# Optimization experiments

Measured on AMD Instinct MI355X. Metric: run time of the kernel, lower is better.

The kernel has to match this reference:

```python
import jax, jax.numpy as jnp
import numpy as np

N_NODES = 50000
N_EDGES = 1600000
NEG_SLOPE = 0.2


def setup_inputs() -> dict:
    key = jax.random.key(0)
    ks = jax.random.split(key, 11)
    s = 0.1  # small init scale
    return {
        "x": jax.random.normal(ks[0], (N_NODES, 128), dtype=jnp.float32),
        "edge_index": jax.random.randint(ks[1], (2, N_EDGES), 0, N_NODES, dtype=jnp.int64),
        "W1": jax.random.normal(ks[2], (128, 128), dtype=jnp.float32) * s,
        "att_src1": jax.random.normal(ks[3], (2, 64), dtype=jnp.float32) * s,
        "att_dst1": jax.random.normal(ks[4], (2, 64), dtype=jnp.float32) * s,
        "b1": jax.random.normal(ks[5], (128,), dtype=jnp.float32) * s,
        "W2": jax.random.normal(ks[6], (128, 64), dtype=jnp.float32) * s,
        "att_src2": jax.random.normal(ks[7], (1, 64), dtype=jnp.float32) * s,
        "att_dst2": jax.random.normal(ks[8], (1, 64), dtype=jnp.float32) * s,
        "b2": jax.random.normal(ks[9], (64,), dtype=jnp.float32) * s,
    }


def gat_conv(x, W, a_src, a_dst, bias, src, dst, n_nodes):
    # x: [N, F_in]; W: [F_in, H*C]; a_src/a_dst: [H, C]; bias: [H*C]
    H, C = a_src.shape
    xl = (x @ W).reshape(n_nodes, H, C)                 # [N,H,C]
    alpha_s = jnp.einsum('nhc,hc->nh', xl, a_src)       # [N,H]
    alpha_d = jnp.einsum('nhc,hc->nh', xl, a_dst)       # [N,H]
    e = jax.nn.leaky_relu(alpha_s[src] + alpha_d[dst], NEG_SLOPE)  # [E,H]
    # segment softmax over edges sharing the same destination node
    m = jax.ops.segment_max(e, dst, num_segments=n_nodes)          # [N,H]
    m = jnp.where(jnp.isfinite(m), m, 0.0)
    e = jnp.exp(e - m[dst])
    denom = jax.ops.segment_sum(e, dst, num_segments=n_nodes)      # [N,H]
    alpha = e / denom[dst]                               # self-loops guarantee denom > 0
    msg = xl[src] * alpha[:, :, None]                    # [E,H,C]
    out = jax.ops.segment_sum(msg, dst, num_segments=n_nodes)      # [N,H,C]
    return out.reshape(n_nodes, H * C) + bias


def reference(x, edge_index, W1, att_src1, att_dst1, b1, W2, att_src2, att_dst2, b2):
    n = x.shape[0]
    # PyG GATConv default add_self_loops=True
    loops = jnp.arange(n, dtype=edge_index.dtype)
    src = jnp.concatenate([edge_index[0], loops])
    dst = jnp.concatenate([edge_index[1], loops])

    h = gat_conv(x, W1, att_src1, att_dst1, b1, src, dst, n)   # [N, 128]
    h = jax.nn.relu(h)                                          # dropout p=0 (eval)
    h = gat_conv(h, W2, att_src2, att_dst2, b2, src, dst, n)   # [N, 64]
    h = jax.nn.relu(h)
    return h
```

## Files before the change

### kernel.cpp

```cpp
#include <hip/hip_runtime.h>
#include <hip/hip_fp16.h>
#include <cstdint>
#include <cstddef>

#define NEG_SLOPE 0.2f

#define NB 128
#define LOG_NB 7
#define MAXK 512

__device__ inline unsigned short f2bf(float f) {
    unsigned int u = __float_as_uint(f);
    u += 0x7FFFu + ((u >> 16) & 1u);
    return (unsigned short)(u >> 16);
}
__device__ inline float bf_lo(unsigned int u) { return __uint_as_float(u << 16); }
__device__ inline float bf_hi(unsigned int u) { return __uint_as_float(u & 0xFFFF0000u); }
__device__ inline float bfu(unsigned short u) { return __uint_as_float((unsigned int)u << 16); }
__device__ inline float lrelu(float t) { return t > 0.f ? t : NEG_SLOPE * t; }

__global__ __launch_bounds__(256) void sort_count_kernel(const int* __restrict__ ei, int E,
                                                         int K, int CH, int* __restrict__ bcnt) {
    __shared__ int hist[4 * MAXK];
    int tid = threadIdx.x;
    int wiw = tid >> 6;
    for (int i = tid; i < K; i += 256) {
        hist[i] = 0; hist[MAXK + i] = 0; hist[2 * MAXK + i] = 0; hist[3 * MAXK + i] = 0;
    }
    __syncthreads();
    int lo = blockIdx.x * CH;
    int hi = lo + CH; if (hi > E) hi = E;
    for (int e = lo + tid; e < hi; e += 256)
        atomicAdd(&hist[wiw * MAXK + (ei[(size_t)E + e] >> LOG_NB)], 1);
    __syncthreads();
    for (int i = tid; i < K; i += 256) {
        int c = hist[i] + hist[MAXK + i] + hist[2 * MAXK + i] + hist[3 * MAXK + i];
        if (c) atomicAdd(&bcnt[i], c);
    }
}

__global__ void sort_scan_kernel(const int* __restrict__ bcnt, int* __restrict__ boff,
                                 int* __restrict__ bcur, int K, int E) {
    __shared__ int buf[MAXK];
    int tid = threadIdx.x;
    int v = (tid < K) ? bcnt[tid] : 0;
    buf[tid] = v;
    __syncthreads();
    for (int o = 1; o < MAXK; o <<= 1) {
        int t = (tid >= o) ? buf[tid - o] : 0;
        __syncthreads();
        buf[tid] += t;
        __syncthreads();
    }
    if (tid < K) {
        int ex = buf[tid] - v;
        boff[tid] = ex;
        bcur[tid] = ex;
    }
    if (tid == K) boff[K] = E;
}


template <int FOUT, int H, int ROWS, bool BF16IN, bool CHUNK_OUT>
__device__ __forceinline__ void gemm_att_body(const void* __restrict__ Xv,
                                              const float* __restrict__ W,
                                              const float* __restrict__ attS,
                                              const float* __restrict__ attD,
                                              unsigned short* __restrict__ Ybf,
                                              float* __restrict__ as_,
                                              float* __restrict__ ad_, int N, int bid,
                                              float* sX, float* sW) {
    constexpr int CG  = FOUT / 4;
    constexpr int RR  = (ROWS * FOUT) / 1024;
    constexpr int LDX = 36;
    int tid = threadIdx.x;
    int rowbase = bid * ROWS;
    int cg = tid % CG;
    int rg = tid / CG;
    int r0 = rg * RR;

    float acc[RR][4];
#pragma unroll
    for (int i = 0; i < RR; i++)
#pragma unroll
        for (int c = 0; c < 4; c++) acc[i][c] = 0.f;

    for (int k0 = 0; k0 < 128; k0 += 32) {
        __syncthreads();
        for (int idx = tid; idx < ROWS * 8; idx += 256) {
            int r = idx >> 3, q = idx & 7;
            int row = rowbase + r;
            float4 val;
            if (row < N) {
                if constexpr (BF16IN) {
                    const unsigned short* Xb = (const unsigned short*)Xv;
                    ushort4 raw = *(const ushort4*)&Xb[(size_t)row * 128 + k0 + q * 4];
                    val = make_float4(bfu(raw.x), bfu(raw.y), bfu(raw.z), bfu(raw.w));
                } else {
                    const float* X = (const float*)Xv;
                    val = *(const float4*)&X[(size_t)row * 128 + k0 + q * 4];
                }
            } else {
                val = make_float4(0.f, 0.f, 0.f, 0.f);
            }
            *(float4*)&sX[r * LDX + q * 4] = val;
        }
        for (int idx = tid; idx < 8 * FOUT; idx += 256)
            *(float4*)&sW[idx * 4] = *(const float4*)&W[(size_t)k0 * FOUT + idx * 4];
        __syncthreads();
        for (int k = 0; k < 32; k += 4) {
            float4 xr[RR];
#pragma unroll
            for (int i = 0; i < RR; i++)
                xr[i] = *(const float4*)&sX[(r0 + i) * LDX + k];
#pragma unroll
            for (int kk = 0; kk < 4; kk++) {
                float4 wv = ((const float4*)(sW + (size_t)(k + kk) * FOUT))[cg];
#pragma unroll
                for (int i = 0; i < RR; i++) {
                    float xv = (&xr[i].x)[kk];
                    acc[i][0] = fmaf(xv, wv.x, acc[i][0]);
                    acc[i][1] = fmaf(xv, wv.y, acc[i][1]);
                    acc[i][2] = fmaf(xv, wv.z, acc[i][2]);
                    acc[i][3] = fmaf(xv, wv.w, acc[i][3]);
                }
            }
        }
    }

#pragma unroll
    for (int i = 0; i < RR; i++) {
        int row = rowbase + r0 + i;
        if (row < N) {
            ushort4 v;
            v.x = f2bf(acc[i][0]); v.y = f2bf(acc[i][1]);
            v.z = f2bf(acc[i][2]); v.w = f2bf(acc[i][3]);
            if constexpr (CHUNK_OUT) {
                int chunk = cg >> 3;
                int wc = (cg & 7) * 4;
                *(ushort4*)(Ybf + ((size_t)chunk * N + row) * 32 + wc) = v;
            } else {
                *(ushort4*)(Ybf + (size_t)row * FOUT + cg * 4) = v;
            }
        }
    }

    float4 asv = ((const float4*)attS)[cg];
    float4 adv = ((const float4*)attD)[cg];
    int head = (H == 2) ? (cg >> 4) : 0;
#pragma unroll
    for (int i = 0; i < RR; i++) {
        float ps = acc[i][0] * asv.x + acc[i][1] * asv.y + acc[i][2] * asv.z + acc[i][3] * asv.w;
        float pd = acc[i][0] * adv.x + acc[i][1] * adv.y + acc[i][2] * adv.z + acc[i][3] * adv.w;
#pragma unroll
        for (int o = 1; o <= 8; o <<= 1) { ps += __shfl_xor(ps, o); pd += __shfl_xor(pd, o); }
        int row = rowbase + r0 + i;
        if ((tid & 15) == 0 && row < N) {
            as_[(size_t)row * H + head] = ps;
            ad_[(size_t)row * H + head] = pd;
        }
    }
}

__global__ __launch_bounds__(256) void scatter_gemm1_kernel(const int* __restrict__ ei, int E,
                                                            int K, int CH, int* __restrict__ bcur,
                                                            unsigned int* __restrict__ bkt,
                                                            const float* __restrict__ X,
                                                            const float* __restrict__ W1,
                                                            const float* __restrict__ attS,
                                                            const float* __restrict__ attD,
                                                            unsigned short* __restrict__ Ybf,
                                                            float* __restrict__ as_,
                                                            float* __restrict__ ad_, int N, int G) {
    __shared__ float sX[64 * 36];
    __shared__ float sW[32 * 128];
    if (blockIdx.x < G) {
        int* hist = (int*)sX;
        int* base = (int*)sW;
        int* cur2 = (int*)sW + MAXK;
        int tid = threadIdx.x;
        int wiw = tid >> 6;
        for (int i = tid; i < K; i += 256) {
            hist[i] = 0; hist[MAXK + i] = 0; hist[2 * MAXK + i] = 0; hist[3 * MAXK + i] = 0;
        }
        __syncthreads();
        int lo = blockIdx.x * CH;
        int hi = lo + CH; if (hi > E) hi = E;
        for (int e = lo + tid; e < hi; e += 256)
            atomicAdd(&hist[wiw * MAXK + (ei[(size_t)E + e] >> LOG_NB)], 1);
        __syncthreads();
        for (int i = tid; i < K; i += 256) {
            int c = hist[i] + hist[MAXK + i] + hist[2 * MAXK + i] + hist[3 * MAXK + i];
            base[i] = c ? atomicAdd(&bcur[i], c) : 0;
            cur2[i] = 0;
        }
        __syncthreads();
        for (int e = lo + tid; e < hi; e += 256) {
            int s = ei[e];
            int d = ei[(size_t)E + e];
            int k = d >> LOG_NB;
            int r = atomicAdd(&cur2[k], 1);
            bkt[(size_t)base[k] + r] = (unsigned int)s | ((unsigned int)d << 16);
        }
    } else {
        gemm_att_body<128, 2, 64, false, true>(X, W1, attS, attD, Ybf, as_, ad_, N,
                                               blockIdx.x - G, sX, sW);
    }
}

__global__ __launch_bounds__(256) void gemm2_kernel(const unsigned short* __restrict__ X,
                                                    const float* __restrict__ W,
                                                    const float* __restrict__ attS,
                                                    const float* __restrict__ attD,
                                                    unsigned short* __restrict__ Ybf,
                                                    float* __restrict__ as_,
                                                    float* __restrict__ ad_, int N) {
    __shared__ float sX[64 * 36];
    __shared__ float sW[32 * 64];
    gemm_att_body<64, 1, 64, true, false>(X, W, attS, attD, Ybf, as_, ad_, N, blockIdx.x, sX, sW);
}

__global__ __launch_bounds__(256) void sort_finalize_kernel(const unsigned int* __restrict__ bkt,
                                                            const int* __restrict__ boff,
                                                            int* __restrict__ off,
                                                            unsigned int* __restrict__ csrc, int N) {
    __shared__ int nhist[4 * NB];
    __shared__ int part[256];
    __shared__ int loff[NB];
    int k = blockIdx.x;
    int tid = threadIdx.x;
    int wiw = tid >> 6;
    int node0 = k << LOG_NB;
    int nh = N - node0; if (nh > NB) nh = NB;
    int beg = boff[k], end = boff[k + 1];
    for (int i = tid; i < NB; i += 256) {
        nhist[i] = 0; nhist[NB + i] = 0; nhist[2 * NB + i] = 0; nhist[3 * NB + i] = 0;
    }
    __syncthreads();
    for (int e = beg + tid; e < end; e += 256)
        atomicAdd(&nhist[wiw * NB + ((bkt[e] >> 16) - node0)], 1);
    __syncthreads();
    int i0 = 2 * tid, i1 = 2 * tid + 1;
    int v0 = (i0 < nh) ? nhist[i0] + nhist[NB + i0] + nhist[2 * NB + i0] + nhist[3 * NB + i0] + 1 : 0;
    int v1 = (i1 < nh) ? nhist[i1] + nhist[NB + i1] + nhist[2 * NB + i1] + nhist[3 * NB + i1] + 1 : 0;
    part[tid] = v0 + v1;
    __syncthreads();
    for (int o = 1; o < 256; o <<= 1) {
        int t = (tid >= o) ? part[tid - o] : 0;
        __syncthreads();
        part[tid] += t;
        __syncthreads();
    }
    int gbase = beg + node0;
    int base = gbase + ((tid > 0) ? part[tid - 1] : 0);
    if (i0 < nh) loff[i0] = base;
    if (i1 < nh) loff[i1] = base + v0;
    __syncthreads();
    for (int i = tid; i < nh; i += 256) {
        int node = node0 + i;
        off[node] = loff[i];
        csrc[loff[i]] = (unsigned int)node | ((unsigned int)node << 16);
        nhist[i] = loff[i] + 1;
    }
    if (node0 + nh == N && tid == 0) off[N] = gbase + part[255];
    __syncthreads();
    for (int e = beg + tid; e < end; e += 256) {
        unsigned int p = bkt[e];
        int pos = atomicAdd(&nhist[(p >> 16) - node0], 1);
        csrc[pos] = p;
    }
}


__global__ __launch_bounds__(256) void alpha1_kernel(const float* __restrict__ as_,
                                                     const float* __restrict__ ad_,
                                                     const int* __restrict__ off,
                                                     const unsigned int* __restrict__ csrc,
                                                     unsigned int* __restrict__ pae0,
                                                     unsigned int* __restrict__ pae1, int N) {
    int wiw  = threadIdx.x >> 6;
    int lane = threadIdx.x & 63;
    int node = blockIdx.x * 4 + wiw;
    if (node >= N) return;
    int beg = off[node], end = off[node + 1];
    int deg = end - beg;
    float2 adn = ((const float2*)ad_)[node];
    (void)wiw;

    if (deg <= 64) {
        int s = 0;
        float t0 = -1e30f, t1 = -1e30f;
        if (lane < deg) {
            s = (int)(csrc[beg + lane] & 0xFFFFu);
            float2 asv = ((const float2*)as_)[s];
            t0 = lrelu(asv.x + adn.x);
            t1 = lrelu(asv.y + adn.y);
        }
        float m0 = t0, m1 = t1;
#pragma unroll
        for (int o = 32; o; o >>= 1) {
            m0 = fmaxf(m0, __shfl_xor(m0, o));
            m1 = fmaxf(m1, __shfl_xor(m1, o));
        }
        float e0 = (lane < deg) ? __expf(t0 - m0) : 0.f;
        float e1 = (lane < deg) ? __expf(t1 - m1) : 0.f;
        float s0 = e0, s1 = e1;
#pragma unroll
        for (int o = 32; o; o >>= 1) { s0 += __shfl_xor(s0, o); s1 += __shfl_xor(s1, o); }
        if (lane < deg) {
            unsigned int h0 = (unsigned int)__half_as_ushort(__float2half(e0 / s0));
            unsigned int h1 = (unsigned int)__half_as_ushort(__float2half(e1 / s1));
            pae0[beg + lane] = (unsigned int)s | (h0 << 16);
            pae1[beg + lane] = (unsigned int)s | (h1 << 16);
        }
    } else {
        float m0 = -1e30f, m1 = -1e30f;
        for (int b = beg; b < end; b += 64) {
            int e = b + lane;
            if (e < end) {
                int s = (int)(csrc[e] & 0xFFFFu);
                float2 asv = ((const float2*)as_)[s];
                m0 = fmaxf(m0, lrelu(asv.x + adn.x));
                m1 = fmaxf(m1, lrelu(asv.y + adn.y));
            }
        }
#pragma unroll
        for (int o = 32; o; o >>= 1) {
            m0 = fmaxf(m0, __shfl_xor(m0, o));
            m1 = fmaxf(m1, __shfl_xor(m1, o));
        }
        float s0 = 0.f, s1 = 0.f;
        for (int b = beg; b < end; b += 64) {
            int e = b + lane;
            if (e < end) {
                int s = (int)(csrc[e] & 0xFFFFu);
                float2 asv = ((const float2*)as_)[s];
                s0 += __expf(lrelu(asv.x + adn.x) - m0);
                s1 += __expf(lrelu(asv.y + adn.y) - m1);
            }
        }
#pragma unroll
        for (int o = 32; o; o >>= 1) { s0 += __shfl_xor(s0, o); s1 += __shfl_xor(s1, o); }
        float i0 = 1.f / s0, i1 = 1.f / s1;
        for (int b = beg; b < end; b += 64) {
            int e = b + lane;
            if (e < end) {
                int s = (int)(csrc[e] & 0xFFFFu);
                float2 asv = ((const float2*)as_)[s];
                float a0 = __expf(lrelu(asv.x + adn.x) - m0) * i0;
                float a1 = __expf(lrelu(asv.y + adn.y) - m1) * i1;
                unsigned int h0 = (unsigned int)__half_as_ushort(__float2half(a0));
                unsigned int h1 = (unsigned int)__half_as_ushort(__float2half(a1));
                pae0[e] = (unsigned int)s | (h0 << 16);
                pae1[e] = (unsigned int)s | (h1 << 16);
            }
        }
    }
}


__global__ __launch_bounds__(256) void chunk_agg1_kernel(const unsigned short* __restrict__ xlc,
                                                         const unsigned int* __restrict__ pae0,
                                                         const unsigned int* __restrict__ pae1,
                                                         const float* __restrict__ bias,
                                                         const int* __restrict__ off,
                                                         unsigned short* __restrict__ out,
                                                         int N) {
    int bid   = blockIdx.x;
    int slot  = bid & 7;
    int chunk = slot & 3;
    int half  = slot >> 2;
    int blkin = (bid >> 3) * 2 + half;
    int wiw   = threadIdx.x >> 6;
    int lane  = threadIdx.x & 63;
    int node  = blkin * 4 + wiw;
    if (node >= N) return;

    int beg = off[node];
    int deg = off[node + 1] - beg;
    int le = lane >> 2;
    int li = lane & 3;

    const unsigned int* pae = (chunk & 2) ? pae1 : pae0;
    const char* xb = (const char*)xlc + ((size_t)chunk * N) * 64 + li * 16;

    float acc[8];
#pragma unroll
    for (int i = 0; i < 8; i++) acc[i] = 0.f;

    int rounds = (deg + 15) >> 4;
#pragma unroll 4
    for (int r = 0; r < rounds; r++) {
        int e = r * 16 + le;
        unsigned int p = (e < deg) ? pae[beg + e] : 0u;
        float a = __half2float(__ushort_as_half((unsigned short)(p >> 16)));
        int s = (int)(p & 0xFFFFu);
        uint4 v = *(const uint4*)(xb + ((size_t)s << 6));
        acc[0] = fmaf(a, bf_lo(v.x), acc[0]); acc[1] = fmaf(a, bf_hi(v.x), acc[1]);
        acc[2] = fmaf(a, bf_lo(v.y), acc[2]); acc[3] = fmaf(a, bf_hi(v.y), acc[3]);
        acc[4] = fmaf(a, bf_lo(v.z), acc[4]); acc[5] = fmaf(a, bf_hi(v.z), acc[5]);
        acc[6] = fmaf(a, bf_lo(v.w), acc[6]); acc[7] = fmaf(a, bf_hi(v.w), acc[7]);
    }
#pragma unroll
    for (int o = 4; o <= 32; o <<= 1)
#pragma unroll
        for (int i = 0; i < 8; i++) acc[i] += __shfl_xor(acc[i], o);

    if (lane < 4) {
        const float* bp = bias + chunk * 32 + lane * 8;
        unsigned int w0 = (unsigned int)f2bf(fmaxf(acc[0] + bp[0], 0.f)) |
                          ((unsigned int)f2bf(fmaxf(acc[1] + bp[1], 0.f)) << 16);
        unsigned int w1 = (unsigned int)f2bf(fmaxf(acc[2] + bp[2], 0.f)) |
                          ((unsigned int)f2bf(fmaxf(acc[3] + bp[3], 0.f)) << 16);
        unsigned int w2 = (unsigned int)f2bf(fmaxf(acc[4] + bp[4], 0.f)) |
                          ((unsigned int)f2bf(fmaxf(acc[5] + bp[5], 0.f)) << 16);
        unsigned int w3 = (unsigned int)f2bf(fmaxf(acc[6] + bp[6], 0.f)) |
                          ((unsigned int)f2bf(fmaxf(acc[7] + bp[7], 0.f)) << 16);
        *(uint4*)(out + (size_t)node * 128 + chunk * 32 + lane * 8) = make_uint4(w0, w1, w2, w3);
    }
}


__global__ __launch_bounds__(256) void agg2_kernel(const unsigned short* __restrict__ xl,
                                                   const float* __restrict__ as_,
                                                   const float* __restrict__ ad_,
                                                   const float* __restrict__ bias,
                                                   const int* __restrict__ off,
                                                   const unsigned int* __restrict__ csrc,
                                                   float* __restrict__ out, int N) {
    __shared__ float2 sps[4][64];
    int wiw  = threadIdx.x >> 6;
    int lane = threadIdx.x & 63;
    int node = blockIdx.x * 4 + wiw;
    if (node >= N) return;
    int beg = off[node], end = off[node + 1];
    int deg = end - beg;
    float adn = ad_[node];

    int cl  = lane & 7;
    int sub = lane >> 3;
    float acc[8];
#pragma unroll
    for (int i = 0; i < 8; i++) acc[i] = 0.f;
    const char* xbase = (const char*)xl + cl * 16;

    if (deg <= 64) {
        int so = 0;
        float t = -1e30f;
        if (lane < deg) {
            int s = (int)(csrc[beg + lane] & 0xFFFFu);
            so = s << 7;
            t = as_[s] + adn;
            t = t > 0.f ? t : NEG_SLOPE * t;
        }
        float m = t;
#pragma unroll
        for (int o = 32; o; o >>= 1) m = fmaxf(m, __shfl_xor(m, o));
        float evv = (lane < deg) ? __expf(t - m) : 0.f;
        float sum = evv;
#pragma unroll
        for (int o = 32; o; o >>= 1) sum += __shfl_xor(sum, o);
        sps[wiw][lane] = make_float2(evv / sum, __int_as_float(so));
        int iters = (deg + 7) >> 3;
#pragma unroll 8
        for (int j = 0; j < iters; j++) {
            float2 q = sps[wiw][j * 8 + sub];
            float a  = q.x;
            uint4 v  = *(const uint4*)(xbase + __float_as_int(q.y));
            acc[0] = fmaf(a, bf_lo(v.x), acc[0]); acc[1] = fmaf(a, bf_hi(v.x), acc[1]);
            acc[2] = fmaf(a, bf_lo(v.y), acc[2]); acc[3] = fmaf(a, bf_hi(v.y), acc[3]);
            acc[4] = fmaf(a, bf_lo(v.z), acc[4]); acc[5] = fmaf(a, bf_hi(v.z), acc[5]);
            acc[6] = fmaf(a, bf_lo(v.w), acc[6]); acc[7] = fmaf(a, bf_hi(v.w), acc[7]);
        }
    } else {
        float m = -1e30f;
        for (int b = beg; b < end; b += 64) {
            int e = b + lane;
            if (e < end) {
                float t = as_[csrc[e] & 0xFFFFu] + adn;
                t = t > 0.f ? t : NEG_SLOPE * t;
                m = fmaxf(m, t);
            }
        }
#pragma unroll
        for (int o = 32; o; o >>= 1) m = fmaxf(m, __shfl_xor(m, o));
        float sum = 0.f;
        for (int b = beg; b < end; b += 64) {
            int e = b + lane;
            if (e < end) {
                float t = as_[csrc[e] & 0xFFFFu] + adn;
                t = t > 0.f ? t : NEG_SLOPE * t;
                sum += __expf(t - m);
            }
        }
#pragma unroll
        for (int o = 32; o; o >>= 1) sum += __shfl_xor(sum, o);
        float inv = 1.f / sum;
        for (int b = beg; b < end; b += 64) {
            int cnt = end - b; if (cnt > 64) cnt = 64;
            float p = 0.f; int so = 0;
            if (lane < cnt) {
                int s = (int)(csrc[b + lane] & 0xFFFFu);
                so = s << 7;
                float t = as_[s] + adn;
                t = t > 0.f ? t : NEG_SLOPE * t;
                p = __expf(t - m) * inv;
            }
            sps[wiw][lane] = make_float2(p, __int_as_float(so));
            int iters = (cnt + 7) >> 3;
#pragma unroll 8
            for (int j = 0; j < iters; j++) {
                float2 q = sps[wiw][j * 8 + sub];
                float a  = q.x;
                uint4 v  = *(const uint4*)(xbase + __float_as_int(q.y));
                acc[0] = fmaf(a, bf_lo(v.x), acc[0]); acc[1] = fmaf(a, bf_hi(v.x), acc[1]);
                acc[2] = fmaf(a, bf_lo(v.y), acc[2]); acc[3] = fmaf(a, bf_hi(v.y), acc[3]);
                acc[4] = fmaf(a, bf_lo(v.z), acc[4]); acc[5] = fmaf(a, bf_hi(v.z), acc[5]);
                acc[6] = fmaf(a, bf_lo(v.w), acc[6]); acc[7] = fmaf(a, bf_hi(v.w), acc[7]);
            }
        }
    }
#pragma unroll
    for (int o = 8; o <= 32; o <<= 1)
#pragma unroll
        for (int i = 0; i < 8; i++) acc[i] += __shfl_xor(acc[i], o);
    if (sub == 0) {
        float* op = out + (size_t)node * 64 + cl * 8;
        const float* bp = bias + cl * 8;
#pragma unroll
        for (int i = 0; i < 8; i++) op[i] = fmaxf(acc[i] + bp[i], 0.f);
    }
}


extern "C" void kernel_launch(void* const* d_in, const int* in_sizes, int n_in,
                              void* d_out, int out_size, void* d_ws, size_t ws_size,
                              hipStream_t stream) {
    const float* x        = (const float*)d_in[0];
    const int*   ei       = (const int*)d_in[1];
    const float* W1       = (const float*)d_in[2];
    const float* attS1    = (const float*)d_in[3];
    const float* attD1    = (const float*)d_in[4];
    const float* b1       = (const float*)d_in[5];
    const float* W2       = (const float*)d_in[6];
    const float* attS2    = (const float*)d_in[7];
    const float* attD2    = (const float*)d_in[8];
    const float* b2       = (const float*)d_in[9];
    float* out            = (float*)d_out;

    int N  = in_sizes[0] / 128;
    int E  = in_sizes[1] / 2;
    int EE = E + N;
    int K  = (N + NB - 1) >> LOG_NB;

    char* w = (char*)d_ws;
    auto alloc = [&](size_t bytes) -> void* {
        void* p = (void*)w;
        w += (bytes + 255) & ~(size_t)255;
        return p;
    };
    int*   bcnt = (int*)alloc((size_t)(K + 1) * 4);
    int*   boff = (int*)alloc((size_t)(K + 1) * 4);
    int*   bcur = (int*)alloc((size_t)(K + 1) * 4);
    int*   off  = (int*)alloc((size_t)(N + 1) * 4);
    unsigned int* csrc = (unsigned int*)alloc((size_t)EE * 4);
    unsigned int* bkt  = (unsigned int*)alloc((size_t)E * 4);
    unsigned short* xl1 = (unsigned short*)alloc((size_t)N * 128 * 2);
    float* sd1  = (float*)alloc((size_t)N * 2 * 4);
    float* dd1  = (float*)alloc((size_t)N * 2 * 4);
    unsigned short* h1 = (unsigned short*)alloc((size_t)N * 128 * 2);
    unsigned int* pae0 = (unsigned int*)alloc((size_t)EE * 4);
    unsigned int* pae1 = (unsigned int*)alloc((size_t)EE * 4);

    unsigned short* xl2 = xl1;
    float* sd2 = sd1;
    float* dd2 = dd1;

    hipMemsetAsync(bcnt, 0, (size_t)(K + 1) * 4, stream);

    int G   = 256;
    int CH  = (E + G - 1) / G;
    int GB1 = (N + 63) / 64;
    sort_count_kernel<<<G, 256, 0, stream>>>(ei, E, K, CH, bcnt);
    sort_scan_kernel<<<1, MAXK, 0, stream>>>(bcnt, boff, bcur, K, E);
    scatter_gemm1_kernel<<<G + GB1, 256, 0, stream>>>(ei, E, K, CH, bcur, bkt,
                                                      x, W1, attS1, attD1, xl1, sd1, dd1, N, G);
    sort_finalize_kernel<<<K, 256, 0, stream>>>(bkt, boff, off, csrc, N);

    alpha1_kernel<<<(N + 3) / 4, 256, 0, stream>>>(sd1, dd1, off, csrc, pae0, pae1, N);
    int CAB = ((N + 7) / 8) * 8;
    chunk_agg1_kernel<<<CAB, 256, 0, stream>>>(xl1, pae0, pae1, b1, off, h1, N);

    gemm2_kernel<<<(N + 63) / 64, 256, 0, stream>>>(h1, W2, attS2, attD2, xl2, sd2, dd2, N);
    agg2_kernel<<<(N + 3) / 4, 256, 0, stream>>>(xl2, sd2, dd2, b2, off, csrc, out, N);
}
```

Before: 339.3 us.

## Pack four nodes per wavefront in layer-1 aggregation and loop alpha over nodes

The layer-1 chunked aggregation now gives each node 16 lanes instead of a whole wavefront, so four destination nodes share one wavefront and the cross-lane reduction shrinks. The loop trip count is the maximum degree among the packed nodes, which adds some divergence waste when degrees differ. The alpha kernel has each wavefront walk 8 consecutive nodes, cutting the grid size by eight. The small-degree path of the layer-2 aggregation is manually unrolled by four so more gathers are in flight at once.

```diff
diff --git a/kernel.cpp b/kernel.cpp
--- a/kernel.cpp
+++ b/kernel.cpp
@@ -18,6 +18,12 @@
 __device__ inline float bf_hi(unsigned int u) { return __uint_as_float(u & 0xFFFF0000u); }
 __device__ inline float bfu(unsigned short u) { return __uint_as_float((unsigned int)u << 16); }
 __device__ inline float lrelu(float t) { return t > 0.f ? t : NEG_SLOPE * t; }
+
+#define FMA8(a, v)                                                                       \
+    acc[0] = fmaf(a, bf_lo((v).x), acc[0]); acc[1] = fmaf(a, bf_hi((v).x), acc[1]);      \
+    acc[2] = fmaf(a, bf_lo((v).y), acc[2]); acc[3] = fmaf(a, bf_hi((v).y), acc[3]);      \
+    acc[4] = fmaf(a, bf_lo((v).z), acc[4]); acc[5] = fmaf(a, bf_hi((v).z), acc[5]);      \
+    acc[6] = fmaf(a, bf_lo((v).w), acc[6]); acc[7] = fmaf(a, bf_hi((v).w), acc[7]);
 
 __global__ __launch_bounds__(256) void sort_count_kernel(const int* __restrict__ ei, int E,
                                                          int K, int CH, int* __restrict__ bcnt) {
@@ -280,79 +286,83 @@
                                                      unsigned int* __restrict__ pae1, int N) {
     int wiw  = threadIdx.x >> 6;
     int lane = threadIdx.x & 63;
-    int node = blockIdx.x * 4 + wiw;
-    if (node >= N) return;
-    int beg = off[node], end = off[node + 1];
-    int deg = end - beg;
-    float2 adn = ((const float2*)ad_)[node];
-    (void)wiw;
-
-    if (deg <= 64) {
-        int s = 0;
-        float t0 = -1e30f, t1 = -1e30f;
-        if (lane < deg) {
-            s = (int)(csrc[beg + lane] & 0xFFFFu);
-            float2 asv = ((const float2*)as_)[s];
-            t0 = lrelu(asv.x + adn.x);
-            t1 = lrelu(asv.y + adn.y);
-        }
-        float m0 = t0, m1 = t1;
-#pragma unroll
-        for (int o = 32; o; o >>= 1) {
-            m0 = fmaxf(m0, __shfl_xor(m0, o));
-            m1 = fmaxf(m1, __shfl_xor(m1, o));
-        }
-        float e0 = (lane < deg) ? __expf(t0 - m0) : 0.f;
-        float e1 = (lane < deg) ? __expf(t1 - m1) : 0.f;
-        float s0 = e0, s1 = e1;
-#pragma unroll
-        for (int o = 32; o; o >>= 1) { s0 += __shfl_xor(s0, o); s1 += __shfl_xor(s1, o); }
-        if (lane < deg) {
-            unsigned int h0 = (unsigned int)__half_as_ushort(__float2half(e0 / s0));
-            unsigned int h1 = (unsigned int)__half_as_ushort(__float2half(e1 / s1));
-            pae0[beg + lane] = (unsigned int)s | (h0 << 16);
-            pae1[beg + lane] = (unsigned int)s | (h1 << 16);
-        }
-    } else {
-        float m0 = -1e30f, m1 = -1e30f;
-        for (int b = beg; b < end; b += 64) {
-            int e = b + lane;
-            if (e < end) {
-                int s = (int)(csrc[e] & 0xFFFFu);
+    int nbase = (blockIdx.x * 4 + wiw) * 8;
+    if (nbase >= N) return;
+
+    for (int k = 0; k < 8; k++) {
+        int node = nbase + k;
+        if (node >= N) break;
+        int beg = off[node], end = off[node + 1];
+        int deg = end - beg;
+        float2 adn = ((const float2*)ad_)[node];
+
+        if (deg <= 64) {
+            int s = 0;
+            float t0 = -1e30f, t1 = -1e30f;
+            if (lane < deg) {
+                s = (int)(csrc[beg + lane] & 0xFFFFu);
                 float2 asv = ((const float2*)as_)[s];
-                m0 = fmaxf(m0, lrelu(asv.x + adn.x));
-                m1 = fmaxf(m1, lrelu(asv.y + adn.y));
-            }
-        }
-#pragma unroll
-        for (int o = 32; o; o >>= 1) {
-            m0 = fmaxf(m0, __shfl_xor(m0, o));
-            m1 = fmaxf(m1, __shfl_xor(m1, o));
-        }
-        float s0 = 0.f, s1 = 0.f;
-        for (int b = beg; b < end; b += 64) {
-            int e = b + lane;
-            if (e < end) {
-                int s = (int)(csrc[e] & 0xFFFFu);
-                float2 asv = ((const float2*)as_)[s];
-                s0 += __expf(lrelu(asv.x + adn.x) - m0);
-                s1 += __expf(lrelu(asv.y + adn.y) - m1);
-            }
-        }
-#pragma unroll
-        for (int o = 32; o; o >>= 1) { s0 += __shfl_xor(s0, o); s1 += __shfl_xor(s1, o); }
-        float i0 = 1.f / s0, i1 = 1.f / s1;
-        for (int b = beg; b < end; b += 64) {
-            int e = b + lane;
-            if (e < end) {
-                int s = (int)(csrc[e] & 0xFFFFu);
-                float2 asv = ((const float2*)as_)[s];
-                float a0 = __expf(lrelu(asv.x + adn.x) - m0) * i0;
-                float a1 = __expf(lrelu(asv.y + adn.y) - m1) * i1;
-                unsigned int h0 = (unsigned int)__half_as_ushort(__float2half(a0));
-                unsigned int h1 = (unsigned int)__half_as_ushort(__float2half(a1));
-                pae0[e] = (unsigned int)s | (h0 << 16);
-                pae1[e] = (unsigned int)s | (h1 << 16);
+                t0 = lrelu(asv.x + adn.x);
+                t1 = lrelu(asv.y + adn.y);
+            }
+            float m0 = t0, m1 = t1;
+#pragma unroll
+            for (int o = 32; o; o >>= 1) {
+                m0 = fmaxf(m0, __shfl_xor(m0, o));
+                m1 = fmaxf(m1, __shfl_xor(m1, o));
+            }
+            float e0 = (lane < deg) ? __expf(t0 - m0) : 0.f;
+            float e1 = (lane < deg) ? __expf(t1 - m1) : 0.f;
+            float s0 = e0, s1 = e1;
+#pragma unroll
+            for (int o = 32; o; o >>= 1) { s0 += __shfl_xor(s0, o); s1 += __shfl_xor(s1, o); }
+            if (lane < deg) {
+                unsigned int h0 = (unsigned int)__half_as_ushort(__float2half(e0 / s0));
+                unsigned int h1 = (unsigned int)__half_as_ushort(__float2half(e1 / s1));
+                pae0[beg + lane] = (unsigned int)s | (h0 << 16);
+                pae1[beg + lane] = (unsigned int)s | (h1 << 16);
+            }
+        } else {
+            float m0 = -1e30f, m1 = -1e30f;
+            for (int b = beg; b < end; b += 64) {
+                int e = b + lane;
+                if (e < end) {
+                    int s = (int)(csrc[e] & 0xFFFFu);
+                    float2 asv = ((const float2*)as_)[s];
+                    m0 = fmaxf(m0, lrelu(asv.x + adn.x));
+                    m1 = fmaxf(m1, lrelu(asv.y + adn.y));
+                }
+            }
+#pragma unroll
+            for (int o = 32; o; o >>= 1) {
+                m0 = fmaxf(m0, __shfl_xor(m0, o));
+                m1 = fmaxf(m1, __shfl_xor(m1, o));
+            }
+            float s0 = 0.f, s1 = 0.f;
+            for (int b = beg; b < end; b += 64) {
+                int e = b + lane;
+                if (e < end) {
+                    int s = (int)(csrc[e] & 0xFFFFu);
+                    float2 asv = ((const float2*)as_)[s];
+                    s0 += __expf(lrelu(asv.x + adn.x) - m0);
+                    s1 += __expf(lrelu(asv.y + adn.y) - m1);
+                }
+            }
+#pragma unroll
+            for (int o = 32; o; o >>= 1) { s0 += __shfl_xor(s0, o); s1 += __shfl_xor(s1, o); }
+            float i0 = 1.f / s0, i1 = 1.f / s1;
+            for (int b = beg; b < end; b += 64) {
+                int e = b + lane;
+                if (e < end) {
+                    int s = (int)(csrc[e] & 0xFFFFu);
+                    float2 asv = ((const float2*)as_)[s];
+                    float a0 = __expf(lrelu(asv.x + adn.x) - m0) * i0;
+                    float a1 = __expf(lrelu(asv.y + adn.y) - m1) * i1;
+                    unsigned int h0 = (unsigned int)__half_as_ushort(__float2half(a0));
+                    unsigned int h1 = (unsigned int)__half_as_ushort(__float2half(a1));
+                    pae0[e] = (unsigned int)s | (h0 << 16);
+                    pae1[e] = (unsigned int)s | (h1 << 16);
+                }
             }
         }
     }
@@ -373,13 +383,19 @@
     int blkin = (bid >> 3) * 2 + half;
     int wiw   = threadIdx.x >> 6;
     int lane  = threadIdx.x & 63;
-    int node  = blkin * 4 + wiw;
-    if (node >= N) return;
-
-    int beg = off[node];
-    int deg = off[node + 1] - beg;
-    int le = lane >> 2;
-    int li = lane & 3;
+    int node  = blkin * 16 + wiw * 4 + (lane >> 4);
+    int l16   = lane & 15;
+    int esub  = l16 >> 2;
+    int li    = l16 & 3;
+
+    bool valid = node < N;
+    int beg = 0, deg = 0;
+    if (valid) { beg = off[node]; deg = off[node + 1] - beg; }
+
+    int md = deg;
+    md = max(md, __shfl_xor(md, 16));
+    md = max(md, __shfl_xor(md, 32));
+    int iters = (md + 3) >> 2;
 
     const unsigned int* pae = (chunk & 2) ? pae1 : pae0;
     const char* xb = (const char*)xlc + ((size_t)chunk * N) * 64 + li * 16;
@@ -388,26 +404,22 @@
 #pragma unroll
     for (int i = 0; i < 8; i++) acc[i] = 0.f;
 
-    int rounds = (deg + 15) >> 4;
-#pragma unroll 4
-    for (int r = 0; r < rounds; r++) {
-        int e = r * 16 + le;
+#pragma unroll 2
+    for (int r = 0; r < iters; r++) {
+        int e = r * 4 + esub;
         unsigned int p = (e < deg) ? pae[beg + e] : 0u;
         float a = __half2float(__ushort_as_half((unsigned short)(p >> 16)));
         int s = (int)(p & 0xFFFFu);
         uint4 v = *(const uint4*)(xb + ((size_t)s << 6));
-        acc[0] = fmaf(a, bf_lo(v.x), acc[0]); acc[1] = fmaf(a, bf_hi(v.x), acc[1]);
-        acc[2] = fmaf(a, bf_lo(v.y), acc[2]); acc[3] = fmaf(a, bf_hi(v.y), acc[3]);
-        acc[4] = fmaf(a, bf_lo(v.z), acc[4]); acc[5] = fmaf(a, bf_hi(v.z), acc[5]);
-        acc[6] = fmaf(a, bf_lo(v.w), acc[6]); acc[7] = fmaf(a, bf_hi(v.w), acc[7]);
-    }
-#pragma unroll
-    for (int o = 4; o <= 32; o <<= 1)
+        FMA8(a, v)
+    }
+#pragma unroll
+    for (int o = 4; o <= 8; o <<= 1)
 #pragma unroll
         for (int i = 0; i < 8; i++) acc[i] += __shfl_xor(acc[i], o);
 
-    if (lane < 4) {
-        const float* bp = bias + chunk * 32 + lane * 8;
+    if (valid && esub == 0) {
+        const float* bp = bias + chunk * 32 + li * 8;
         unsigned int w0 = (unsigned int)f2bf(fmaxf(acc[0] + bp[0], 0.f)) |
                           ((unsigned int)f2bf(fmaxf(acc[1] + bp[1], 0.f)) << 16);
         unsigned int w1 = (unsigned int)f2bf(fmaxf(acc[2] + bp[2], 0.f)) |
@@ -416,7 +428,7 @@
                           ((unsigned int)f2bf(fmaxf(acc[5] + bp[5], 0.f)) << 16);
         unsigned int w3 = (unsigned int)f2bf(fmaxf(acc[6] + bp[6], 0.f)) |
                           ((unsigned int)f2bf(fmaxf(acc[7] + bp[7], 0.f)) << 16);
-        *(uint4*)(out + (size_t)node * 128 + chunk * 32 + lane * 8) = make_uint4(w0, w1, w2, w3);
+        *(uint4*)(out + (size_t)node * 128 + chunk * 32 + li * 8) = make_uint4(w0, w1, w2, w3);
     }
 }
 
@@ -462,15 +474,22 @@
         for (int o = 32; o; o >>= 1) sum += __shfl_xor(sum, o);
         sps[wiw][lane] = make_float2(evv / sum, __int_as_float(so));
         int iters = (deg + 7) >> 3;
-#pragma unroll 8
-        for (int j = 0; j < iters; j++) {
-            float2 q = sps[wiw][j * 8 + sub];
-            float a  = q.x;
+        int g = 0;
+        for (; g + 4 <= iters; g += 4) {
+            float2 q0 = sps[wiw][(g + 0) * 8 + sub];
+            float2 q1 = sps[wiw][(g + 1) * 8 + sub];
+            float2 q2 = sps[wiw][(g + 2) * 8 + sub];
+            float2 q3 = sps[wiw][(g + 3) * 8 + sub];
+            uint4 v0 = *(const uint4*)(xbase + __float_as_int(q0.y));
+            uint4 v1 = *(const uint4*)(xbase + __float_as_int(q1.y));
+            uint4 v2 = *(const uint4*)(xbase + __float_as_int(q2.y));
+            uint4 v3 = *(const uint4*)(xbase + __float_as_int(q3.y));
+            FMA8(q0.x, v0) FMA8(q1.x, v1) FMA8(q2.x, v2) FMA8(q3.x, v3)
+        }
+        for (; g < iters; g++) {
+            float2 q = sps[wiw][g * 8 + sub];
             uint4 v  = *(const uint4*)(xbase + __float_as_int(q.y));
-            acc[0] = fmaf(a, bf_lo(v.x), acc[0]); acc[1] = fmaf(a, bf_hi(v.x), acc[1]);
-            acc[2] = fmaf(a, bf_lo(v.y), acc[2]); acc[3] = fmaf(a, bf_hi(v.y), acc[3]);
-            acc[4] = fmaf(a, bf_lo(v.z), acc[4]); acc[5] = fmaf(a, bf_hi(v.z), acc[5]);
-            acc[6] = fmaf(a, bf_lo(v.w), acc[6]); acc[7] = fmaf(a, bf_hi(v.w), acc[7]);
+            FMA8(q.x, v)
         }
     } else {
         float m = -1e30f;
@@ -513,10 +532,7 @@
                 float2 q = sps[wiw][j * 8 + sub];
                 float a  = q.x;
                 uint4 v  = *(const uint4*)(xbase + __float_as_int(q.y));
-                acc[0] = fmaf(a, bf_lo(v.x), acc[0]); acc[1] = fmaf(a, bf_hi(v.x), acc[1]);
-                acc[2] = fmaf(a, bf_lo(v.y), acc[2]); acc[3] = fmaf(a, bf_hi(v.y), acc[3]);
-                acc[4] = fmaf(a, bf_lo(v.z), acc[4]); acc[5] = fmaf(a, bf_hi(v.z), acc[5]);
-                acc[6] = fmaf(a, bf_lo(v.w), acc[6]); acc[7] = fmaf(a, bf_hi(v.w), acc[7]);
+                FMA8(a, v)
             }
         }
     }
@@ -587,8 +603,9 @@
                                                       x, W1, attS1, attD1, xl1, sd1, dd1, N, G);
     sort_finalize_kernel<<<K, 256, 0, stream>>>(bkt, boff, off, csrc, N);
 
-    alpha1_kernel<<<(N + 3) / 4, 256, 0, stream>>>(sd1, dd1, off, csrc, pae0, pae1, N);
-    int CAB = ((N + 7) / 8) * 8;
+    alpha1_kernel<<<(N + 31) / 32, 256, 0, stream>>>(sd1, dd1, off, csrc, pae0, pae1, N);
+    int NG  = (N + 15) / 16;
+    int CAB = ((NG + 1) / 2) * 8;
     chunk_agg1_kernel<<<CAB, 256, 0, stream>>>(xl1, pae0, pae1, b1, off, h1, N);
 
     gemm2_kernel<<<(N + 63) / 64, 256, 0, stream>>>(h1, W2, attS2, attD2, xl2, sd2, dd2, N);
```

Result: faster. 292.2 us (-13.9%).
